# Performance work log

Measured on AMD Instinct MI355X. Metric: run time of the kernel, lower is better.

The kernel has to match this reference:

```python
import jax, jax.numpy as jnp
import numpy as np

FP8_E4M3_MAX = 448.0  # max_value for fp8 e4m3fn in the torch module


def _to_fp8_e4m3(x):
    # round-to-nearest fp8 e4m3fn values, represented back in fp32
    return x.astype(jnp.float8_e4m3fn).astype(jnp.float32)


def setup_inputs() -> dict:
    key = jax.random.key(0)
    k1, k2, k3 = jax.random.split(key, 3)
    B, S, K, N = 4, 2048, 4096, 14336
    x = jax.random.normal(k1, (B, S, K), dtype=jnp.float32)
    # per-tensor scales (QParamsLinear enforces per_tensor qscheme for this path)
    weight_scale = jnp.array([0.01], dtype=jnp.float32)
    input_scale = jnp.array([0.02], dtype=jnp.float32)
    # weight stored in real-quantized fp8 form (values are exact e4m3 lattice points)
    w_fp = jax.random.normal(k2, (N, K), dtype=jnp.float32)
    weight_q = _to_fp8_e4m3(jnp.clip(w_fp / weight_scale, -FP8_E4M3_MAX, FP8_E4M3_MAX))
    bias = jax.random.normal(k3, (N,), dtype=jnp.float32)
    return {"x": x, "weight_q": weight_q, "weight_scale": weight_scale,
            "input_scale": input_scale, "bias": bias}


def reference(x, weight_q, weight_scale, input_scale, bias):
    # Quantize activation: divide by per-tensor scale, clamp to fp8 range, cast to e4m3
    qx = jnp.clip(x / input_scale, -FP8_E4M3_MAX, FP8_E4M3_MAX)
    qx = qx.astype(jnp.float8_e4m3fn).astype(x.dtype)
    # scaled_mm: (qx @ weight_q.T) * (input_scale * weight_scale) + bias
    out = jnp.einsum("bsk,nk->bsn", qx, weight_q.astype(x.dtype))
    out = out * (input_scale * weight_scale)[0] + bias
    return out
```

## Files before the change

### kernel.cpp

```cpp
#include <hip/hip_runtime.h>
#include <stdint.h>

typedef float f32x4  __attribute__((ext_vector_type(4)));
typedef float f32x16 __attribute__((ext_vector_type(16)));
typedef int   i32x4  __attribute__((ext_vector_type(4)));
typedef int   i32x8  __attribute__((ext_vector_type(8)));

constexpr int Mdim = 8192;
constexpr int Ndim = 14336;
constexpr int Kdim = 4096;
constexpr int BM = 256, BN = 256, BK = 64;
constexpr int NT = Kdim / BK;
constexpr uint32_t SLOT = 32768;

#define VMCNT(n) asm volatile("s_waitcnt vmcnt(" #n ")" ::: "memory")
#define LGKM(n)  do { asm volatile("s_waitcnt lgkmcnt(" #n ")" ::: "memory"); \
                      __builtin_amdgcn_sched_barrier(0); } while (0)
#define BARRIER() do { asm volatile("" ::: "memory"); \
                       __builtin_amdgcn_s_barrier(); \
                       asm volatile("" ::: "memory"); } while (0)

__device__ __forceinline__ void gload_lds16(const void* g, void* l) {
  __builtin_amdgcn_global_load_lds(
      (const __attribute__((address_space(1))) unsigned int*)g,
      (__attribute__((address_space(3))) unsigned int*)l, 16, 0, 0);
}

__device__ __forceinline__ i32x4 ldsr128(const uint8_t* p) {
  i32x4 r;
  asm volatile("ds_read_b128 %0, %1"
               : "=v"(r)
               : "v"((const __attribute__((address_space(3))) uint8_t*)p));
  return r;
}

__device__ __forceinline__ i32x8 frag(const uint8_t* tile, int row, int kh) {
  const int p0 = (kh * 32) ^ (((row >> 1) & 3) << 4);
  const uint8_t* rp = tile + row * 64;
  i32x4 lo = ldsr128(rp + p0);
  i32x4 hi = ldsr128(rp + (p0 ^ 16));
  return __builtin_shufflevector(lo, hi, 0, 1, 2, 3, 4, 5, 6, 7);
}

__device__ __forceinline__ f32x16 mx(i32x8 a, i32x8 b, f32x16 c) {
  return __builtin_amdgcn_mfma_scale_f32_32x32x64_f8f6f4(
      a, b, c, 0, 0, 0, 0x7f7f7f7f, 0, 0x7f7f7f7f);
}

__global__ void __launch_bounds__(256) quant_fp8_kernel(
    const float* __restrict__ in, uint8_t* __restrict__ out8,
    const float* __restrict__ scale_ptr, long long n)
{
  const float s = scale_ptr ? scale_ptr[0] : 1.0f;
  const long long nch = n >> 3;
  const long long idx = (long long)blockIdx.x * blockDim.x + threadIdx.x;
  const long long stride = (long long)gridDim.x * blockDim.x;
  for (long long c = idx; c < nch; c += stride) {
    f32x4 v0 = *(const f32x4*)(in + c * 8);
    f32x4 v1 = *(const f32x4*)(in + c * 8 + 4);
    float q[8];
#pragma unroll
    for (int j = 0; j < 4; ++j) {
      q[j]     = fminf(fmaxf(v0[j] / s, -448.f), 448.f);
      q[4 + j] = fminf(fmaxf(v1[j] / s, -448.f), 448.f);
    }
    unsigned int w0 = 0, w1 = 0;
    w0 = __builtin_amdgcn_cvt_pk_fp8_f32(q[0], q[1], w0, false);
    w0 = __builtin_amdgcn_cvt_pk_fp8_f32(q[2], q[3], w0, true);
    w1 = __builtin_amdgcn_cvt_pk_fp8_f32(q[4], q[5], w1, false);
    w1 = __builtin_amdgcn_cvt_pk_fp8_f32(q[6], q[7], w1, true);
    uint2 r; r.x = w0; r.y = w1;
    *(uint2*)(out8 + c * 8) = r;
  }
}

__global__ void __launch_bounds__(512, 2) gemm_fp8_kernel(
    const uint8_t* __restrict__ qa, const uint8_t* __restrict__ qb,
    const float* __restrict__ iscale, const float* __restrict__ wscale,
    const float* __restrict__ bias, float* __restrict__ out)
{
  __shared__ uint8_t smem[4 * SLOT];

  const int tid  = threadIdx.x;
  const int wave = tid >> 6;
  const int lane = tid & 63;
  const int wm   = wave >> 2;
  const int wn   = wave & 3;
  const int col  = lane & 31;
  const int kh   = lane >> 5;
  const long long tile_m = (long long)blockIdx.y * BM;
  const long long tile_n = (long long)blockIdx.x * BN;

  const int urow = tid >> 2;
  const int pbs  = tid & 3;
  const int scol = (pbs ^ ((urow >> 1) & 3)) << 4;
  const uint8_t* gA = qa + (tile_m + urow) * Kdim + scol;
  const uint8_t* gB = qb + (tile_n + urow) * Kdim + scol;
  uint8_t* lbase = smem + wave * 1024;

#define STAGE(u, mat, tt, boff)                                            \
  gload_lds16((mat ? gB : gA) + (long long)(u) * 128 * Kdim +              \
                  (long long)(tt) * BK,                                    \
              lbase + (boff) + (mat) * 16384 + (u) * 8192)

  f32x16 acc[4][2] = {};

  const int rowA = wm * 128 + col;
  const int rowB = wn * 64 + col;

#pragma unroll
  for (int tt = 0; tt < 3; ++tt) {
    STAGE(0, 0, tt, (uint32_t)tt * SLOT); STAGE(1, 0, tt, (uint32_t)tt * SLOT);
    STAGE(0, 1, tt, (uint32_t)tt * SLOT); STAGE(1, 1, tt, (uint32_t)tt * SLOT);
  }

  for (int t = 0; t < NT; ++t) {
    const uint8_t* Ab = smem + (uint32_t)(t & 3) * SLOT;
    const uint8_t* Bb = Ab + 16384;

    if (t + 2 < NT)      { VMCNT(8); }
    else if (t + 1 < NT) { VMCNT(4); }
    else                 { VMCNT(0); }
    BARRIER();

    if (t + 3 < NT) {
      const uint32_t bo = (uint32_t)((t + 3) & 3) * SLOT;
      STAGE(0, 0, t + 3, bo); STAGE(1, 0, t + 3, bo);
      STAGE(0, 1, t + 3, bo); STAGE(1, 1, t + 3, bo);
    }

    i32x8 A0 = frag(Ab, rowA +  0, kh);
    i32x8 A1 = frag(Ab, rowA + 32, kh);
    i32x8 B0 = frag(Bb, rowB +  0, kh);
    i32x8 B1 = frag(Bb, rowB + 32, kh);
    i32x8 A2 = frag(Ab, rowA + 64, kh);
    i32x8 A3 = frag(Ab, rowA + 96, kh);

    LGKM(4);
    __builtin_amdgcn_s_setprio(1);
    acc[0][0] = mx(A0, B0, acc[0][0]);  acc[0][1] = mx(A0, B1, acc[0][1]);
    acc[1][0] = mx(A1, B0, acc[1][0]);  acc[1][1] = mx(A1, B1, acc[1][1]);
    __builtin_amdgcn_s_setprio(0);
    LGKM(0);
    __builtin_amdgcn_s_setprio(1);
    acc[2][0] = mx(A2, B0, acc[2][0]);  acc[2][1] = mx(A2, B1, acc[2][1]);
    acc[3][0] = mx(A3, B0, acc[3][0]);  acc[3][1] = mx(A3, B1, acc[3][1]);
    __builtin_amdgcn_s_setprio(0);
  }

  const float alpha = iscale[0] * wscale[0];
  const long long col0 = tile_n + wn * 64 + col;
  const float bv0 = bias[col0];
  const float bv1 = bias[col0 + 32];
#pragma unroll
  for (int m = 0; m < 4; ++m) {
#pragma unroll
    for (int r = 0; r < 16; ++r) {
      const long long row =
          tile_m + wm * 128 + m * 32 + (r & 3) + 8 * (r >> 2) + 4 * kh;
      float* op = out + row * (long long)Ndim + col0;
      op[0]  = acc[m][0][r] * alpha + bv0;
      op[32] = acc[m][1][r] * alpha + bv1;
    }
  }
#undef STAGE
}

extern "C" void kernel_launch(void* const* d_in, const int* in_sizes, int n_in,
                              void* d_out, int out_size, void* d_ws, size_t ws_size,
                              hipStream_t stream) {
  const float* x      = (const float*)d_in[0];
  const float* weight = (const float*)d_in[1];
  const float* wscale = (const float*)d_in[2];
  const float* iscale = (const float*)d_in[3];
  const float* bias   = (const float*)d_in[4];
  float* out = (float*)d_out;

  uint8_t* qx = (uint8_t*)d_ws;
  uint8_t* qw = qx + (long long)Mdim * Kdim;

  const long long nx = (long long)Mdim * Kdim;
  const long long nw = (long long)Ndim * Kdim;

  quant_fp8_kernel<<<4096, 256, 0, stream>>>(x, qx, iscale, nx);
  quant_fp8_kernel<<<4096, 256, 0, stream>>>(weight, qw, nullptr, nw);

  dim3 grid(Ndim / BN, Mdim / BM);
  gemm_fp8_kernel<<<grid, 512, 0, stream>>>(qx, qw, iscale, wscale, bias, out);
}
```

Baseline: 570.2 us.

## Split loop into two barrier-separated halves, fuse quant kernels, nontemporal stores

Merges the two fp8 quantization launches into one kernel that walks both tensors, saving a launch. The GEMM main loop is split into two phases separated by an extra barrier: the A halves are staged after the first four fragment reads and the B halves after the second, interleaving global->LDS traffic with MFMA work. Output stores become nontemporal to avoid polluting cache. The extra per-iteration barrier and full lgkm waits may reduce overlap, and a sched_barrier is added to vmcnt waits.

```diff
diff --git a/kernel.cpp b/kernel.cpp
--- a/kernel.cpp
+++ b/kernel.cpp
@@ -1,10 +1,11 @@
 #include <hip/hip_runtime.h>
 #include <stdint.h>
 
-typedef float f32x4  __attribute__((ext_vector_type(4)));
-typedef float f32x16 __attribute__((ext_vector_type(16)));
-typedef int   i32x4  __attribute__((ext_vector_type(4)));
-typedef int   i32x8  __attribute__((ext_vector_type(8)));
+typedef float    f32x4  __attribute__((ext_vector_type(4)));
+typedef float    f32x16 __attribute__((ext_vector_type(16)));
+typedef int      i32x4  __attribute__((ext_vector_type(4)));
+typedef int      i32x8  __attribute__((ext_vector_type(8)));
+typedef uint32_t u32x4  __attribute__((ext_vector_type(4)));
 
 constexpr int Mdim = 8192;
 constexpr int Ndim = 14336;
@@ -13,7 +14,8 @@
 constexpr int NT = Kdim / BK;
 constexpr uint32_t SLOT = 32768;
 
-#define VMCNT(n) asm volatile("s_waitcnt vmcnt(" #n ")" ::: "memory")
+#define VMCNT(n) do { asm volatile("s_waitcnt vmcnt(" #n ")" ::: "memory"); \
+                      __builtin_amdgcn_sched_barrier(0); } while (0)
 #define LGKM(n)  do { asm volatile("s_waitcnt lgkmcnt(" #n ")" ::: "memory"); \
                       __builtin_amdgcn_sched_barrier(0); } while (0)
 #define BARRIER() do { asm volatile("" ::: "memory"); \
@@ -34,30 +36,30 @@
   return r;
 }
 
-__device__ __forceinline__ i32x8 frag(const uint8_t* tile, int row, int kh) {
-  const int p0 = (kh * 32) ^ (((row >> 1) & 3) << 4);
-  const uint8_t* rp = tile + row * 64;
-  i32x4 lo = ldsr128(rp + p0);
-  i32x4 hi = ldsr128(rp + (p0 ^ 16));
-  return __builtin_shufflevector(lo, hi, 0, 1, 2, 3, 4, 5, 6, 7);
-}
-
 __device__ __forceinline__ f32x16 mx(i32x8 a, i32x8 b, f32x16 c) {
   return __builtin_amdgcn_mfma_scale_f32_32x32x64_f8f6f4(
       a, b, c, 0, 0, 0, 0x7f7f7f7f, 0, 0x7f7f7f7f);
 }
 
-__global__ void __launch_bounds__(256) quant_fp8_kernel(
-    const float* __restrict__ in, uint8_t* __restrict__ out8,
-    const float* __restrict__ scale_ptr, long long n)
+__global__ void __launch_bounds__(256) quant_both_kernel(
+    const float* __restrict__ x, const float* __restrict__ w,
+    uint8_t* __restrict__ qx, uint8_t* __restrict__ qw,
+    const float* __restrict__ iscale, long long nx, long long nw)
 {
-  const float s = scale_ptr ? scale_ptr[0] : 1.0f;
-  const long long nch = n >> 3;
+  const float sx = iscale[0];
+  const long long ncx = nx >> 3, ncw = nw >> 3;
+  const long long total = ncx + ncw;
   const long long idx = (long long)blockIdx.x * blockDim.x + threadIdx.x;
   const long long stride = (long long)gridDim.x * blockDim.x;
-  for (long long c = idx; c < nch; c += stride) {
-    f32x4 v0 = *(const f32x4*)(in + c * 8);
-    f32x4 v1 = *(const f32x4*)(in + c * 8 + 4);
+  for (long long c = idx; c < total; c += stride) {
+    const float* in;
+    uint8_t* out8;
+    float s;
+    long long cc;
+    if (c < ncx) { in = x; out8 = qx; s = sx;   cc = c; }
+    else         { in = w; out8 = qw; s = 1.0f; cc = c - ncx; }
+    f32x4 v0 = *(const f32x4*)(in + cc * 8);
+    f32x4 v1 = *(const f32x4*)(in + cc * 8 + 4);
     float q[8];
 #pragma unroll
     for (int j = 0; j < 4; ++j) {
@@ -70,7 +72,7 @@
     w1 = __builtin_amdgcn_cvt_pk_fp8_f32(q[4], q[5], w1, false);
     w1 = __builtin_amdgcn_cvt_pk_fp8_f32(q[6], q[7], w1, true);
     uint2 r; r.x = w0; r.y = w1;
-    *(uint2*)(out8 + c * 8) = r;
+    *(uint2*)(out8 + cc * 8) = r;
   }
 }
 
@@ -103,44 +105,53 @@
                   (long long)(tt) * BK,                                    \
               lbase + (boff) + (mat) * 16384 + (u) * 8192)
 
+#define FRAG64(dst, tile, row)                                             \
+  {                                                                        \
+    const int p0_ = (kh * 32) ^ ((((row) >> 1) & 3) << 4);                 \
+    const uint8_t* rp_ = (tile) + (row) * 64;                              \
+    i32x4 lo_ = ldsr128(rp_ + p0_);                                        \
+    i32x4 hi_ = ldsr128(rp_ + (p0_ ^ 16));                                 \
+    dst = __builtin_shufflevector(lo_, hi_, 0, 1, 2, 3, 4, 5, 6, 7);       \
+  }
+
   f32x16 acc[4][2] = {};
-
   const int rowA = wm * 128 + col;
   const int rowB = wn * 64 + col;
 
 #pragma unroll
   for (int tt = 0; tt < 3; ++tt) {
-    STAGE(0, 0, tt, (uint32_t)tt * SLOT); STAGE(1, 0, tt, (uint32_t)tt * SLOT);
-    STAGE(0, 1, tt, (uint32_t)tt * SLOT); STAGE(1, 1, tt, (uint32_t)tt * SLOT);
+    const uint32_t bo = (uint32_t)tt * SLOT;
+    STAGE(0, 0, tt, bo); STAGE(1, 0, tt, bo);
+    STAGE(0, 1, tt, bo); STAGE(1, 1, tt, bo);
   }
 
   for (int t = 0; t < NT; ++t) {
     const uint8_t* Ab = smem + (uint32_t)(t & 3) * SLOT;
     const uint8_t* Bb = Ab + 16384;
+    const uint32_t bo = (uint32_t)((t + 3) & 3) * SLOT;
 
     if (t + 2 < NT)      { VMCNT(8); }
     else if (t + 1 < NT) { VMCNT(4); }
     else                 { VMCNT(0); }
     BARRIER();
 
-    if (t + 3 < NT) {
-      const uint32_t bo = (uint32_t)((t + 3) & 3) * SLOT;
-      STAGE(0, 0, t + 3, bo); STAGE(1, 0, t + 3, bo);
-      STAGE(0, 1, t + 3, bo); STAGE(1, 1, t + 3, bo);
-    }
-
-    i32x8 A0 = frag(Ab, rowA +  0, kh);
-    i32x8 A1 = frag(Ab, rowA + 32, kh);
-    i32x8 B0 = frag(Bb, rowB +  0, kh);
-    i32x8 B1 = frag(Bb, rowB + 32, kh);
-    i32x8 A2 = frag(Ab, rowA + 64, kh);
-    i32x8 A3 = frag(Ab, rowA + 96, kh);
-
-    LGKM(4);
+    i32x8 A0, A1, B0, B1;
+    FRAG64(A0, Ab, rowA +  0);
+    FRAG64(A1, Ab, rowA + 32);
+    FRAG64(B0, Bb, rowB +  0);
+    FRAG64(B1, Bb, rowB + 32);
+    if (t + 3 < NT) { STAGE(0, 0, t + 3, bo); STAGE(1, 0, t + 3, bo); }
+    LGKM(0);
     __builtin_amdgcn_s_setprio(1);
     acc[0][0] = mx(A0, B0, acc[0][0]);  acc[0][1] = mx(A0, B1, acc[0][1]);
     acc[1][0] = mx(A1, B0, acc[1][0]);  acc[1][1] = mx(A1, B1, acc[1][1]);
     __builtin_amdgcn_s_setprio(0);
+    BARRIER();
+
+    i32x8 A2, A3;
+    FRAG64(A2, Ab, rowA + 64);
+    FRAG64(A3, Ab, rowA + 96);
+    if (t + 3 < NT) { STAGE(0, 1, t + 3, bo); STAGE(1, 1, t + 3, bo); }
     LGKM(0);
     __builtin_amdgcn_s_setprio(1);
     acc[2][0] = mx(A2, B0, acc[2][0]);  acc[2][1] = mx(A2, B1, acc[2][1]);
@@ -159,10 +170,11 @@
       const long long row =
           tile_m + wm * 128 + m * 32 + (r & 3) + 8 * (r >> 2) + 4 * kh;
       float* op = out + row * (long long)Ndim + col0;
-      op[0]  = acc[m][0][r] * alpha + bv0;
-      op[32] = acc[m][1][r] * alpha + bv1;
+      __builtin_nontemporal_store(acc[m][0][r] * alpha + bv0, op);
+      __builtin_nontemporal_store(acc[m][1][r] * alpha + bv1, op + 32);
     }
   }
+#undef FRAG64
 #undef STAGE
 }
 
@@ -182,8 +194,7 @@
   const long long nx = (long long)Mdim * Kdim;
   const long long nw = (long long)Ndim * Kdim;
 
-  quant_fp8_kernel<<<4096, 256, 0, stream>>>(x, qx, iscale, nx);
-  quant_fp8_kernel<<<4096, 256, 0, stream>>>(weight, qw, nullptr, nw);
+  quant_both_kernel<<<4096, 256, 0, stream>>>(x, weight, qx, qw, iscale, nx, nw);
 
   dim3 grid(Ndim / BN, Mdim / BM);
   gemm_fp8_kernel<<<grid, 512, 0, stream>>>(qx, qw, iscale, wscale, bias, out);
```

Result: no change. 560.7 us (-1.7%).
